# Performance work log

Measured on AMD Instinct MI355X. Metric: run time of the kernel, lower is better.

Reference implementation:

```python
import jax, jax.numpy as jnp
import numpy as np

B, N, C = 4, 262144, 10
K_PRE, K_POST = 4096, 500          # before_nms_max, after_nms_max
ROI_THR, NMS_THR = 0.1, 0.01       # roi_threshold, nms_threshold


def setup_inputs() -> dict:
    key = jax.random.key(0)
    k1, k2, k3, k4 = jax.random.split(key, 4)
    # raw logits; sigmoid(-2 + noise) straddles roi_threshold=0.1 realistically
    cls = jax.random.normal(k1, (B, N, C), jnp.float32) - 2.0
    centers = jax.random.uniform(k2, (B, N, 3), jnp.float32, minval=-50.0, maxval=50.0)
    sizes = jax.random.uniform(k3, (B, N, 3), jnp.float32, minval=0.5, maxval=5.0)
    heading = jax.random.uniform(k4, (B, N, 1), jnp.float32, minval=-np.pi, maxval=np.pi)
    boxes = jnp.concatenate([centers, sizes, heading], axis=-1)  # (B, N, 7)
    return {"batch_cls_preds": cls, "batch_box_preds": boxes}


def _pairwise_bev_iou(b):
    # b: (K, 7) = [x, y, z, dx, dy, dz, heading]; BEV IoU (heading ignored,
    # axis-aligned approximation of the rotated-IoU CUDA kernel).
    x, y, dx, dy = b[:, 0], b[:, 1], b[:, 3], b[:, 4]
    x1, x2 = x - dx * 0.5, x + dx * 0.5
    y1, y2 = y - dy * 0.5, y + dy * 0.5
    ix = jnp.clip(jnp.minimum(x2[:, None], x2[None, :]) - jnp.maximum(x1[:, None], x1[None, :]), 0.0)
    iy = jnp.clip(jnp.minimum(y2[:, None], y2[None, :]) - jnp.maximum(y1[:, None], y1[None, :]), 0.0)
    inter = ix * iy                              # (K, K)
    area = dx * dy                               # (K,)
    union = area[:, None] + area[None, :] - inter
    return inter / jnp.maximum(union, 1e-6)


def _nms_one(scores, labels, boxes):
    # scores: (N,), labels: (N,) int32, boxes: (N, 7)
    s = jnp.where(scores > ROI_THR, scores, -1.0)       # score-threshold filter
    topv, topi = jax.lax.top_k(s, K_PRE)                # keep top before_nms_max
    tb = boxes[topi]                                     # (K_PRE, 7)
    tl = labels[topi]
    iou = _pairwise_bev_iou(tb)                          # (K_PRE, K_PRE)
    keep0 = topv > ROI_THR

    def body(i, keep):
        # a kept higher-score box i suppresses later boxes with IoU > thr
        sup = (iou[i] > NMS_THR) & (jnp.arange(K_PRE) > i) & keep[i]
        return keep & ~sup

    keep = jax.lax.fori_loop(0, K_PRE, body, keep0)
    kept_scores = jnp.where(keep, topv, -1.0)
    fv, fi = jax.lax.top_k(kept_scores, K_POST)          # after_nms_max slots
    m = fv > 0.0
    final_scores = jnp.where(m, fv, 0.0)                 # (K_POST,)
    final_boxes = tb[fi] * m[:, None].astype(tb.dtype)   # (K_POST, 7)
    final_labels = jnp.where(m, tl[fi], -1)              # (K_POST,)
    return final_scores, final_boxes, final_labels


def reference(batch_cls_preds, batch_box_preds):
    probs = jax.nn.sigmoid(batch_cls_preds)              # (B, N, C)
    scores = jnp.max(probs, axis=-1)                     # per-anchor best class score
    labels = jnp.argmax(probs, axis=-1).astype(jnp.int32)
    final_scores, final_boxes, final_labels = jax.vmap(_nms_one)(scores, labels, batch_box_preds)
    return final_scores, final_boxes, final_labels
```

## Files before the change

kernel.cpp:

```cpp
#include <hip/hip_runtime.h>
#include <stdint.h>

constexpr int B = 4;
constexpr int N = 262144;
constexpr int C = 10;
constexpr int KPRE = 4096;
constexpr int KPOST = 500;
constexpr float ROI_THR = 0.1f;
constexpr float NMS_THR = 0.01f;
constexpr int CAP = 8192;
constexpr int MASKW = KPRE / 64;
constexpr int RJT = 2;
constexpr int MAXP = 32;

__device__ __forceinline__ uint32_t f2k(float f) {
  uint32_t u = __float_as_uint(f);
  return (u & 0x80000000u) ? ~u : (u | 0x80000000u);
}
__device__ __forceinline__ float k2f(uint32_t k) {
  uint32_t u = (k & 0x80000000u) ? (k ^ 0x80000000u) : ~k;
  return __uint_as_float(u);
}
__device__ __forceinline__ float sigm(float x) { return 1.0f / (1.0f + expf(-x)); }

__device__ __forceinline__ void async_lds16(const void* g, void* l) {
  __builtin_amdgcn_global_load_lds((const __attribute__((address_space(1))) void*)g,
                                   (__attribute__((address_space(3))) void*)l, 16, 0, 0);
}

__device__ __forceinline__ uint2 select256(const uint32_t* __restrict__ h, uint32_t R,
                                           uint32_t* s, uint32_t* o2) {
  int t = threadIdx.x;
  s[t] = h[t];
  __syncthreads();
  for (int off = 1; off < 256; off <<= 1) {
    uint32_t v = s[t] + ((t + off < 256) ? s[t + off] : 0u);
    __syncthreads();
    s[t] = v;
    __syncthreads();
  }
  uint32_t suf = s[t];
  uint32_t sufn = (t < 255) ? s[t + 1] : 0u;
  if (suf >= R && R > sufn) {
    o2[0] = (uint32_t)t;
    o2[1] = R - sufn;
  }
  __syncthreads();
  uint2 r;
  r.x = o2[0];
  r.y = o2[1];
  __syncthreads();
  return r;
}

__global__ void zeroK(uint32_t* __restrict__ p, int n) {
  int i = blockIdx.x * 256 + threadIdx.x;
  if (i < n) p[i] = 0u;
}

__global__ void scoreK(const float* __restrict__ cls, uint32_t* __restrict__ keys,
                       uint32_t* __restrict__ hist0, uint32_t* __restrict__ hist1) {
  __shared__ float ls[2560];
  __shared__ uint32_t h[256];
  __shared__ uint32_t h1[256];
  int b = blockIdx.y;
  int t = threadIdx.x;
  h[t] = 0;
  h1[t] = 0;
  size_t base = ((size_t)b * N + (size_t)blockIdx.x * 256) * C;
  const float2* g2 = (const float2*)(cls + base);
  float2* l2 = (float2*)ls;
#pragma unroll
  for (int r = 0; r < 5; ++r) l2[r * 256 + t] = g2[r * 256 + t];
  __syncthreads();
  const float* mine = ls + t * 10;
  float m = mine[0];
#pragma unroll
  for (int c = 1; c < C; ++c) m = fmaxf(m, mine[c]);
  float p = sigm(m);
  float sc = (p > ROI_THR) ? p : -1.0f;
  uint32_t k = f2k(sc);
  keys[(size_t)b * N + blockIdx.x * 256 + t] = k;
  atomicAdd(&h[k >> 24], 1u);
  if ((k >> 24) == 0xBFu) atomicAdd(&h1[(k >> 16) & 255u], 1u);
  __syncthreads();
  if (h[t]) atomicAdd(&hist0[b * 256 + t], h[t]);
  if (h1[t]) atomicAdd(&hist1[b * 256 + t], h1[t]);
}

__global__ void histP1K(const uint32_t* __restrict__ keys, const uint32_t* __restrict__ hist0,
                        uint32_t* __restrict__ hist1b) {
  __shared__ uint32_t s[256];
  __shared__ uint32_t o2[2];
  __shared__ uint32_t h[256];
  int b = blockIdx.y;
  int t = threadIdx.x;
  uint2 s0 = select256(hist0 + b * 256, (uint32_t)KPRE, s, o2);
  if (s0.x == 0xBFu) return;
  h[t] = 0;
  __syncthreads();
  uint32_t pref = s0.x;
  const uint4* kb4 = (const uint4*)(keys + (size_t)b * N);
#pragma unroll
  for (int r = 0; r < 2; ++r) {
    uint4 kv = kb4[blockIdx.x * 512 + r * 256 + t];
#pragma unroll
    for (int j = 0; j < 4; ++j) {
      uint32_t k = (&kv.x)[j];
      if ((k >> 24) == pref) atomicAdd(&h[(k >> 16) & 255u], 1u);
    }
  }
  __syncthreads();
  if (h[t]) atomicAdd(&hist1b[b * 256 + t], h[t]);
}

__global__ void compactK(const uint32_t* __restrict__ keys, const uint32_t* __restrict__ hist0,
                         const uint32_t* __restrict__ hist1, const uint32_t* __restrict__ hist1b,
                         unsigned long long* __restrict__ list, uint32_t* __restrict__ cnt) {
  __shared__ uint32_t s[256];
  __shared__ uint32_t o2[2];
  __shared__ uint32_t scan[256];
  __shared__ uint32_t baseSh;
  int b = blockIdx.y;
  int t = threadIdx.x;
  uint2 s0 = select256(hist0 + b * 256, (uint32_t)KPRE, s, o2);
  const uint32_t* h1 = (s0.x == 0xBFu) ? hist1 : hist1b;
  uint2 s1 = select256(h1 + b * 256, s0.y, s, o2);
  uint32_t T = ((s0.x << 8) | s1.x) << 16;
  const uint4* kb4 = (const uint4*)(keys + (size_t)b * N);
  uint4 kv[4];
#pragma unroll
  for (int r = 0; r < 4; ++r) kv[r] = kb4[blockIdx.x * 1024 + r * 256 + t];
  uint32_t c = 0;
#pragma unroll
  for (int r = 0; r < 4; ++r)
#pragma unroll
    for (int j = 0; j < 4; ++j) c += ((&kv[r].x)[j] >= T) ? 1u : 0u;
  scan[t] = c;
  __syncthreads();
  for (int off = 1; off < 256; off <<= 1) {
    uint32_t v = scan[t] + ((t >= off) ? scan[t - off] : 0u);
    __syncthreads();
    scan[t] = v;
    __syncthreads();
  }
  uint32_t excl = scan[t] - c;
  if (t == 255) baseSh = atomicAdd(&cnt[b], scan[255]);
  __syncthreads();
  uint32_t pos = baseSh + excl;
#pragma unroll
  for (int r = 0; r < 4; ++r)
#pragma unroll
    for (int j = 0; j < 4; ++j) {
      uint32_t k = (&kv[r].x)[j];
      if (k >= T) {
        uint32_t n = (blockIdx.x * 1024 + r * 256 + t) * 4 + j;
        if (pos < CAP)
          list[(size_t)b * CAP + pos] = ((unsigned long long)k << 32) | (uint32_t)(~n);
        pos++;
      }
    }
}

__global__ void rankK(const unsigned long long* __restrict__ list, const uint32_t* __restrict__ cnt,
                      uint32_t* __restrict__ rank) {
  __shared__ unsigned long long lp[256];
  int b = blockIdx.z;
  int cc = (int)min(cnt[b], (uint32_t)CAP);
  if (blockIdx.x * 256 >= cc) return;
  int j0 = blockIdx.y * (256 * RJT);
  if (j0 >= cc) return;
  int i = blockIdx.x * 256 + threadIdx.x;
  unsigned long long pi = (i < cc) ? list[(size_t)b * CAP + i] : ~0ull;
  uint32_t c = 0;
#pragma unroll
  for (int tb = 0; tb < RJT; ++tb) {
    int j = j0 + tb * 256 + threadIdx.x;
    __syncthreads();
    lp[threadIdx.x] = (j < cc) ? list[(size_t)b * CAP + j] : 0ull;
    __syncthreads();
#pragma unroll 8
    for (int jj = 0; jj < 256; ++jj) c += (lp[jj] > pi) ? 1u : 0u;
  }
  if (i < cc && c) atomicAdd(&rank[(size_t)b * CAP + i], c);
}

__global__ void scatterK(const unsigned long long* __restrict__ list,
                         const uint32_t* __restrict__ cnt, const uint32_t* __restrict__ rank,
                         const float* __restrict__ boxes, float* __restrict__ sel_score,
                         uint32_t* __restrict__ sel_idx, float* __restrict__ sel_box) {
  int b = blockIdx.y;
  int p = blockIdx.x * 256 + threadIdx.x;
  uint32_t cc = min(cnt[b], (uint32_t)CAP);
  if (p >= (int)cc) return;
  unsigned long long pk = list[(size_t)b * CAP + p];
  uint32_t r = rank[(size_t)b * CAP + p];
  if (r >= (uint32_t)KPRE) return;
  uint32_t key = (uint32_t)(pk >> 32);
  uint32_t idx = ~(uint32_t)pk;
  sel_score[b * KPRE + r] = k2f(key);
  sel_idx[b * KPRE + r] = idx;
  const float* src = boxes + ((size_t)b * N + idx) * 7;
  float* dst = sel_box + ((size_t)b * KPRE + r) * 8;
#pragma unroll
  for (int c = 0; c < 7; ++c) dst[c] = src[c];
  dst[7] = 0.f;
}

template <bool CHK>
__device__ __forceinline__ void mask_row64(int tt, const float4* __restrict__ jv,
                                           const float* __restrict__ ja, float x1i, float x2i,
                                           float y1i, float y2i, float ai, uint32_t& lo0,
                                           uint32_t& hi0, uint32_t& band) {
#pragma unroll 16
  for (int jj = 0; jj < 64; ++jj) {
    float4 v = jv[jj];
    float aj = ja[jj];
    float xx1 = fmaxf(x1i, v.x), xx2 = fminf(x2i, v.y);
    float yy1 = fmaxf(y1i, v.z), yy2 = fminf(y2i, v.w);
    float ix = fmaxf(__fsub_rn(xx2, xx1), 0.0f), iy = fmaxf(__fsub_rn(yy2, yy1), 0.0f);
    float inter = __fmul_rn(ix, iy);
    float den = fmaxf(__fsub_rn(__fadd_rn(ai, aj), inter), 1e-6f);
    float q0 = __fmul_rn(NMS_THR, den);
    float d = __fsub_rn(inter, q0);
    band |= (fabsf(d) <= __fmul_rn(q0, 1e-5f)) ? 1u : 0u;
    bool sup = d > 0.0f;
    if (CHK) sup = sup && (jj > tt);
    uint32_t bit = sup ? 1u : 0u;
    if (jj < 32) lo0 |= bit << jj; else hi0 |= bit << (jj - 32);
  }
}

__global__ __launch_bounds__(64) void maskK(const float* __restrict__ sel_box,
                                            unsigned long long* __restrict__ maskT,
                                            unsigned long long* __restrict__ Tmat) {
  int b = blockIdx.z;
  int bi = blockIdx.x;
  int w = blockIdx.y;
  if (w < bi) return;
  int t = threadIdx.x;
  int i = bi * 64 + t;
  int j0 = w * 64;
  __shared__ float4 jv[64];
  __shared__ float ja[64];
  {
    const float4* bj = (const float4*)(sel_box + ((size_t)b * KPRE + j0 + t) * 8);
    float4 lo = bj[0], hi = bj[1];
    float xj = lo.x, yj = lo.y, dxj = lo.w, dyj = hi.x;
    float hxj = __fmul_rn(dxj, 0.5f), hyj = __fmul_rn(dyj, 0.5f);
    float4 v;
    v.x = __fsub_rn(xj, hxj);
    v.y = __fadd_rn(xj, hxj);
    v.z = __fsub_rn(yj, hyj);
    v.w = __fadd_rn(yj, hyj);
    jv[t] = v;
    ja[t] = __fmul_rn(dxj, dyj);
  }
  __syncthreads();
  const float4* myb = (const float4*)(sel_box + ((size_t)b * KPRE + i) * 8);
  float4 lo = myb[0], hi = myb[1];
  float x = lo.x, y = lo.y, dx = lo.w, dy = hi.x;
  float hx = __fmul_rn(dx, 0.5f), hy = __fmul_rn(dy, 0.5f);
  float x1i = __fsub_rn(x, hx), x2i = __fadd_rn(x, hx);
  float y1i = __fsub_rn(y, hy), y2i = __fadd_rn(y, hy);
  float ai = __fmul_rn(dx, dy);
  uint32_t lo0 = 0, hi0 = 0, band = 0;
  if (w == bi)
    mask_row64<true>(t, jv, ja, x1i, x2i, y1i, y2i, ai, lo0, hi0, band);
  else
    mask_row64<false>(t, jv, ja, x1i, x2i, y1i, y2i, ai, lo0, hi0, band);
  if (__builtin_expect(__any(band != 0), 0)) {
    lo0 = hi0 = 0;
    for (int jj = 0; jj < 64; ++jj) {
      float4 v = jv[jj];
      float aj = ja[jj];
      float xx1 = fmaxf(x1i, v.x), xx2 = fminf(x2i, v.y);
      float yy1 = fmaxf(y1i, v.z), yy2 = fminf(y2i, v.w);
      float ix = fmaxf(__fsub_rn(xx2, xx1), 0.0f), iy = fmaxf(__fsub_rn(yy2, yy1), 0.0f);
      float inter = __fmul_rn(ix, iy);
      float den = fmaxf(__fsub_rn(__fadd_rn(ai, aj), inter), 1e-6f);
      bool sup = (inter / den) > NMS_THR && (j0 + jj > i);
      uint32_t bit = sup ? 1u : 0u;
      if (jj < 32) lo0 |= bit << jj; else hi0 |= bit << (jj - 32);
    }
  }
  unsigned long long wacc = ((unsigned long long)hi0 << 32) | lo0;
  maskT[((size_t)b * MASKW + w) * KPRE + i] = wacc;
  if (w == bi) {
    unsigned long long m = wacc;
    unsigned long long T = 0ull;
#pragma unroll
    for (int j = 0; j < 64; ++j) {
      unsigned long long bj = __ballot(((m >> j) & 1ull) != 0ull);
      if (t == j) T = bj;
    }
    unsigned long long* trow = Tmat + ((size_t)b * 64 + w) * 128;
    trow[t] = T;
    trow[64 + t] = m;
  }
}

__global__ void nmsK(const unsigned long long* __restrict__ maskT,
                     const unsigned long long* __restrict__ Tmat,
                     const float* __restrict__ sel_score,
                     uint32_t* __restrict__ kept_pos, uint32_t* __restrict__ kept_cnt) {
  __shared__ unsigned long long td[64][128];
  __shared__ uint32_t keptbuf[KPOST];
  int b = blockIdx.x;
  int t = threadIdx.x;

  const char* tsrc = (const char*)(Tmat + (size_t)b * 64 * 128);
  for (int g = 0; g < 64; ++g)
    async_lds16(tsrc + (size_t)g * 1024 + (size_t)t * 16, &td[g][0]);

  unsigned long long cand = 0ull;
  for (int k = 0; k < 64; ++k) {
    float s = sel_score[b * KPRE + k * 64 + t];
    unsigned long long bal = __ballot(s > ROI_THR);
    if (t == k) cand = bal;
  }
  asm volatile("s_waitcnt vmcnt(0)" ::: "memory");

  const unsigned long long* mbt = maskT + (size_t)b * KPRE * MASKW + (size_t)t * KPRE;
  unsigned long long remv = 0ull;
  unsigned long long r[MAXP];
#pragma unroll
  for (int a = 0; a < MAXP; ++a) r[a] = 0ull;
  int kc = 0;

  for (int g = 0; g < 64; ++g) {
#pragma unroll
    for (int a = 0; a < MAXP; ++a) remv |= r[a];

    unsigned long long cw = cand & ~remv;
    unsigned long long aw =
        ((unsigned long long)(uint32_t)__builtin_amdgcn_readlane((uint32_t)(cw >> 32), g) << 32) |
        (uint32_t)__builtin_amdgcn_readlane((uint32_t)cw, g);
    if (aw) {
      unsigned long long T = td[g][t];
      unsigned long long m = td[g][64 + t];
      unsigned long long K = __ballot((m & aw) != 0ull);
      unsigned long long alive = aw;
      unsigned long long rem = aw & K;
      if (rem) {
        bool deadf = ((aw >> t) & 1ull) == 0ull;
        while (rem) {
          int s = __ffsll((long long)rem) - 1;
          rem &= rem - 1ull;
          if ((alive >> s) & 1ull) {
            deadf = deadf || (((T >> s) & 1ull) != 0ull);
            alive = __ballot(!deadf);
            rem &= alive;
          }
        }
      }
      int grp = __popcll(alive);
      if ((alive >> t) & 1ull) {
        int rk = __popcll(alive & ((1ull << t) - 1ull));
        if (kc + rk < KPOST) keptbuf[kc + rk] = (uint32_t)(g * 64 + t);
      }
      kc += grp;
      unsigned long long a2 = alive;
      bool again = true;
      while (again) {
#pragma unroll
        for (int a = 0; a < MAXP; ++a) {
          if (a2) {
            int s2 = __ffsll((long long)a2) - 1;
            a2 &= a2 - 1ull;
            r[a] = (t >= g) ? mbt[g * 64 + s2] : 0ull;
          } else {
            r[a] = 0ull;
          }
        }
        if (a2) {
#pragma unroll
          for (int a = 0; a < MAXP; ++a) {
            remv |= r[a];
            r[a] = 0ull;
          }
          again = true;
        } else {
          again = false;
        }
      }
      if (kc >= KPOST) break;
    } else {
#pragma unroll
      for (int a = 0; a < MAXP; ++a) r[a] = 0ull;
    }
  }
  asm volatile("s_waitcnt vmcnt(0)" ::: "memory");
  int kcc = min(kc, KPOST);
  for (int i = t; i < kcc; i += 64) kept_pos[b * KPOST + i] = keptbuf[i];
  if (t == 0) kept_cnt[b] = (uint32_t)kcc;
}

__global__ void outK(const float* __restrict__ cls,
                     const float* __restrict__ sel_score, const uint32_t* __restrict__ sel_idx,
                     const float* __restrict__ sel_box,
                     const uint32_t* __restrict__ kept_pos, const uint32_t* __restrict__ kept_cnt,
                     float* __restrict__ out) {
  int b = blockIdx.y;
  int s = blockIdx.x * blockDim.x + threadIdx.x;
  if (s >= KPOST) return;
  float* oS = out;
  float* oB = out + B * KPOST;
  float* oL = out + B * KPOST + B * KPOST * 7;
  uint32_t kcnt = kept_cnt[b];
  if (s < (int)kcnt) {
    uint32_t pos = kept_pos[b * KPOST + s];
    oS[b * KPOST + s] = sel_score[b * KPRE + pos];
    const float* box = sel_box + ((size_t)b * KPRE + pos) * 8;
    float* dst = oB + ((size_t)b * KPOST + s) * 7;
#pragma unroll
    for (int c = 0; c < 7; ++c) dst[c] = box[c];
    uint32_t idx = sel_idx[b * KPRE + pos];
    const float* p = cls + ((size_t)b * N + idx) * C;
    float bestv = sigm(p[0]);
    int bestc = 0;
#pragma unroll
    for (int c = 1; c < C; ++c) {
      float v = sigm(p[c]);
      if (v > bestv) { bestv = v; bestc = c; }
    }
    oL[b * KPOST + s] = (float)bestc;
  } else {
    oS[b * KPOST + s] = 0.0f;
    float* dst = oB + ((size_t)b * KPOST + s) * 7;
#pragma unroll
    for (int c = 0; c < 7; ++c) dst[c] = 0.0f;
    oL[b * KPOST + s] = -1.0f;
  }
}

__global__ void sentinelK(float* out, int n) {
  int i = blockIdx.x * blockDim.x + threadIdx.x;
  if (i < n) out[i] = 1337.0f;
}

extern "C" void kernel_launch(void* const* d_in, const int* in_sizes, int n_in,
                              void* d_out, int out_size, void* d_ws, size_t ws_size,
                              hipStream_t stream) {
  const float* cls = (const float*)d_in[0];
  const float* boxes = (const float*)d_in[1];
  float* out = (float*)d_out;

  char* ws = (char*)d_ws;
  size_t off = 0;
  auto alloc = [&](size_t bytes) -> void* {
    void* p = ws + off;
    off = (off + bytes + 255) & ~(size_t)255;
    return p;
  };
  size_t mask_bytes = (size_t)B * KPRE * MASKW * 8;
  unsigned long long* mask = (unsigned long long*)alloc(mask_bytes);
  unsigned long long* list = (unsigned long long*)alloc((size_t)B * CAP * 8);
  uint32_t* keys = (uint32_t*)alloc((size_t)B * N * 4);
  float* sel_box = (float*)alloc((size_t)B * KPRE * 8 * 4);
  float* sel_score = (float*)alloc((size_t)B * KPRE * 4);
  uint32_t* sel_idx = (uint32_t*)alloc((size_t)B * KPRE * 4);
  uint32_t* kept_pos = (uint32_t*)alloc((size_t)B * KPOST * 4);
  uint32_t* kept_cnt = (uint32_t*)alloc(B * 4);
  unsigned long long* Tmat = (unsigned long long*)alloc((size_t)B * 64 * 128 * 8);

  uint32_t* hist0 = (uint32_t*)mask;
  uint32_t* hist1 = hist0 + B * 256;
  uint32_t* hist1b = hist1 + B * 256;
  uint32_t* cnt = hist1b + B * 256;
  uint32_t* rank = (uint32_t*)((char*)mask + 16384);
  int zwords = (16384 + B * CAP * 4) / 4;

  if (off > ws_size) {
    sentinelK<<<dim3((out_size + 255) / 256), 256, 0, stream>>>(out, out_size);
    return;
  }

  zeroK<<<dim3((zwords + 255) / 256), 256, 0, stream>>>((uint32_t*)mask, zwords);
  scoreK<<<dim3(N / 256, B), 256, 0, stream>>>(cls, keys, hist0, hist1);
  histP1K<<<dim3(N / 2048, B), 256, 0, stream>>>(keys, hist0, hist1b);
  compactK<<<dim3(N / 4096, B), 256, 0, stream>>>(keys, hist0, hist1, hist1b, list, cnt);
  rankK<<<dim3(CAP / 256, CAP / (256 * RJT), B), 256, 0, stream>>>(list, cnt, rank);
  scatterK<<<dim3(CAP / 256, B), 256, 0, stream>>>(list, cnt, rank, boxes, sel_score, sel_idx,
                                                   sel_box);
  maskK<<<dim3(64, 64, B), 64, 0, stream>>>(sel_box, mask, Tmat);
  nmsK<<<B, 64, 0, stream>>>(mask, Tmat, sel_score, kept_pos, kept_cnt);
  outK<<<dim3((KPOST + 255) / 256, B), 256, 0, stream>>>(cls, sel_score, sel_idx, sel_box,
                                                         kept_pos, kept_cnt, out);
}
```

Before: 150.9 us.

## Fuse rank with scatter via last-block counter, fold output into NMS, drop histogram pass

Removes the histP1K second-level histogram pass: when the top radix bucket is not 0xBF, the threshold now uses only the top byte, so more candidates may reach compaction. Rank and scatter are merged into one kernel, where the last j-chunk block for each i-tile (found with an atomic done counter) does the scatter. The output gather is folded into the single-wave-per-batch NMS kernel. The aim is fewer kernel launches and less inter-kernel idle time, at the cost of possible CAP overflow when the coarser threshold is used, and a serial 64-thread output loop.

```diff
diff --git a/kernel.cpp b/kernel.cpp
--- a/kernel.cpp
+++ b/kernel.cpp
@@ -11,6 +11,7 @@
 constexpr int CAP = 8192;
 constexpr int MASKW = KPRE / 64;
 constexpr int RJT = 2;
+constexpr int NJCH = CAP / (256 * RJT);
 constexpr int MAXP = 32;
 
 __device__ __forceinline__ uint32_t f2k(float f) {
@@ -88,34 +89,8 @@
   if (h1[t]) atomicAdd(&hist1[b * 256 + t], h1[t]);
 }
 
-__global__ void histP1K(const uint32_t* __restrict__ keys, const uint32_t* __restrict__ hist0,
-                        uint32_t* __restrict__ hist1b) {
-  __shared__ uint32_t s[256];
-  __shared__ uint32_t o2[2];
-  __shared__ uint32_t h[256];
-  int b = blockIdx.y;
-  int t = threadIdx.x;
-  uint2 s0 = select256(hist0 + b * 256, (uint32_t)KPRE, s, o2);
-  if (s0.x == 0xBFu) return;
-  h[t] = 0;
-  __syncthreads();
-  uint32_t pref = s0.x;
-  const uint4* kb4 = (const uint4*)(keys + (size_t)b * N);
-#pragma unroll
-  for (int r = 0; r < 2; ++r) {
-    uint4 kv = kb4[blockIdx.x * 512 + r * 256 + t];
-#pragma unroll
-    for (int j = 0; j < 4; ++j) {
-      uint32_t k = (&kv.x)[j];
-      if ((k >> 24) == pref) atomicAdd(&h[(k >> 16) & 255u], 1u);
-    }
-  }
-  __syncthreads();
-  if (h[t]) atomicAdd(&hist1b[b * 256 + t], h[t]);
-}
-
 __global__ void compactK(const uint32_t* __restrict__ keys, const uint32_t* __restrict__ hist0,
-                         const uint32_t* __restrict__ hist1, const uint32_t* __restrict__ hist1b,
+                         const uint32_t* __restrict__ hist1,
                          unsigned long long* __restrict__ list, uint32_t* __restrict__ cnt) {
   __shared__ uint32_t s[256];
   __shared__ uint32_t o2[2];
@@ -124,9 +99,13 @@
   int b = blockIdx.y;
   int t = threadIdx.x;
   uint2 s0 = select256(hist0 + b * 256, (uint32_t)KPRE, s, o2);
-  const uint32_t* h1 = (s0.x == 0xBFu) ? hist1 : hist1b;
-  uint2 s1 = select256(h1 + b * 256, s0.y, s, o2);
-  uint32_t T = ((s0.x << 8) | s1.x) << 16;
+  uint32_t T;
+  if (s0.x == 0xBFu) {
+    uint2 s1 = select256(hist1 + b * 256, s0.y, s, o2);
+    T = ((s0.x << 8) | s1.x) << 16;
+  } else {
+    T = s0.x << 24;
+  }
   const uint4* kb4 = (const uint4*)(keys + (size_t)b * N);
   uint4 kv[4];
 #pragma unroll
@@ -162,49 +141,53 @@
     }
 }
 
-__global__ void rankK(const unsigned long long* __restrict__ list, const uint32_t* __restrict__ cnt,
-                      uint32_t* __restrict__ rank) {
+__global__ void rankscatK(const unsigned long long* __restrict__ list,
+                          const uint32_t* __restrict__ cnt, uint32_t* __restrict__ rank,
+                          uint32_t* __restrict__ done, const float* __restrict__ boxes,
+                          float* __restrict__ sel_score, uint32_t* __restrict__ sel_idx,
+                          float* __restrict__ sel_box) {
   __shared__ unsigned long long lp[256];
+  __shared__ uint32_t lastSh;
   int b = blockIdx.z;
+  int itile = blockIdx.x;
+  int t = threadIdx.x;
   int cc = (int)min(cnt[b], (uint32_t)CAP);
-  if (blockIdx.x * 256 >= cc) return;
-  int j0 = blockIdx.y * (256 * RJT);
-  if (j0 >= cc) return;
-  int i = blockIdx.x * 256 + threadIdx.x;
-  unsigned long long pi = (i < cc) ? list[(size_t)b * CAP + i] : ~0ull;
-  uint32_t c = 0;
-#pragma unroll
-  for (int tb = 0; tb < RJT; ++tb) {
-    int j = j0 + tb * 256 + threadIdx.x;
-    __syncthreads();
-    lp[threadIdx.x] = (j < cc) ? list[(size_t)b * CAP + j] : 0ull;
-    __syncthreads();
+  int i = itile * 256 + t;
+  if (itile * 256 < cc) {
+    int j0 = blockIdx.y * (256 * RJT);
+    if (j0 < cc) {
+      unsigned long long pi = (i < cc) ? list[(size_t)b * CAP + i] : ~0ull;
+      uint32_t c = 0;
+#pragma unroll
+      for (int tb = 0; tb < RJT; ++tb) {
+        int j = j0 + tb * 256 + t;
+        __syncthreads();
+        lp[t] = (j < cc) ? list[(size_t)b * CAP + j] : 0ull;
+        __syncthreads();
 #pragma unroll 8
-    for (int jj = 0; jj < 256; ++jj) c += (lp[jj] > pi) ? 1u : 0u;
-  }
-  if (i < cc && c) atomicAdd(&rank[(size_t)b * CAP + i], c);
-}
-
-__global__ void scatterK(const unsigned long long* __restrict__ list,
-                         const uint32_t* __restrict__ cnt, const uint32_t* __restrict__ rank,
-                         const float* __restrict__ boxes, float* __restrict__ sel_score,
-                         uint32_t* __restrict__ sel_idx, float* __restrict__ sel_box) {
-  int b = blockIdx.y;
-  int p = blockIdx.x * 256 + threadIdx.x;
-  uint32_t cc = min(cnt[b], (uint32_t)CAP);
-  if (p >= (int)cc) return;
-  unsigned long long pk = list[(size_t)b * CAP + p];
-  uint32_t r = rank[(size_t)b * CAP + p];
-  if (r >= (uint32_t)KPRE) return;
-  uint32_t key = (uint32_t)(pk >> 32);
-  uint32_t idx = ~(uint32_t)pk;
-  sel_score[b * KPRE + r] = k2f(key);
-  sel_idx[b * KPRE + r] = idx;
-  const float* src = boxes + ((size_t)b * N + idx) * 7;
-  float* dst = sel_box + ((size_t)b * KPRE + r) * 8;
-#pragma unroll
-  for (int c = 0; c < 7; ++c) dst[c] = src[c];
-  dst[7] = 0.f;
+        for (int jj = 0; jj < 256; ++jj) c += (lp[jj] > pi) ? 1u : 0u;
+      }
+      if (i < cc && c) atomicAdd(&rank[(size_t)b * CAP + i], c);
+    }
+  }
+  __syncthreads();
+  if (t == 0) lastSh = atomicAdd(&done[b * 32 + itile], 1u);
+  __syncthreads();
+  if (lastSh == NJCH - 1 && i < cc) {
+    unsigned long long pk = list[(size_t)b * CAP + i];
+    uint32_t r = atomicAdd(&rank[(size_t)b * CAP + i], 0u);
+    if (r < (uint32_t)KPRE) {
+      uint32_t key = (uint32_t)(pk >> 32);
+      uint32_t idx = ~(uint32_t)pk;
+      sel_score[b * KPRE + r] = k2f(key);
+      sel_idx[b * KPRE + r] = idx;
+      const float* src = boxes + ((size_t)b * N + idx) * 7;
+      float* dst = sel_box + ((size_t)b * KPRE + r) * 8;
+#pragma unroll
+      for (int c7 = 0; c7 < 7; ++c7) dst[c7] = src[c7];
+      dst[7] = 0.f;
+    }
+  }
 }
 
 template <bool CHK>
@@ -300,10 +283,12 @@
   }
 }
 
-__global__ void nmsK(const unsigned long long* __restrict__ maskT,
-                     const unsigned long long* __restrict__ Tmat,
-                     const float* __restrict__ sel_score,
-                     uint32_t* __restrict__ kept_pos, uint32_t* __restrict__ kept_cnt) {
+__global__ void nmsoutK(const unsigned long long* __restrict__ maskT,
+                        const unsigned long long* __restrict__ Tmat,
+                        const float* __restrict__ sel_score,
+                        const uint32_t* __restrict__ sel_idx,
+                        const float* __restrict__ sel_box, const float* __restrict__ cls,
+                        float* __restrict__ out) {
   __shared__ unsigned long long td[64][128];
   __shared__ uint32_t keptbuf[KPOST];
   int b = blockIdx.x;
@@ -392,45 +377,35 @@
   }
   asm volatile("s_waitcnt vmcnt(0)" ::: "memory");
   int kcc = min(kc, KPOST);
-  for (int i = t; i < kcc; i += 64) kept_pos[b * KPOST + i] = keptbuf[i];
-  if (t == 0) kept_cnt[b] = (uint32_t)kcc;
-}
-
-__global__ void outK(const float* __restrict__ cls,
-                     const float* __restrict__ sel_score, const uint32_t* __restrict__ sel_idx,
-                     const float* __restrict__ sel_box,
-                     const uint32_t* __restrict__ kept_pos, const uint32_t* __restrict__ kept_cnt,
-                     float* __restrict__ out) {
-  int b = blockIdx.y;
-  int s = blockIdx.x * blockDim.x + threadIdx.x;
-  if (s >= KPOST) return;
+
   float* oS = out;
   float* oB = out + B * KPOST;
   float* oL = out + B * KPOST + B * KPOST * 7;
-  uint32_t kcnt = kept_cnt[b];
-  if (s < (int)kcnt) {
-    uint32_t pos = kept_pos[b * KPOST + s];
-    oS[b * KPOST + s] = sel_score[b * KPRE + pos];
-    const float* box = sel_box + ((size_t)b * KPRE + pos) * 8;
-    float* dst = oB + ((size_t)b * KPOST + s) * 7;
-#pragma unroll
-    for (int c = 0; c < 7; ++c) dst[c] = box[c];
-    uint32_t idx = sel_idx[b * KPRE + pos];
-    const float* p = cls + ((size_t)b * N + idx) * C;
-    float bestv = sigm(p[0]);
-    int bestc = 0;
-#pragma unroll
-    for (int c = 1; c < C; ++c) {
-      float v = sigm(p[c]);
-      if (v > bestv) { bestv = v; bestc = c; }
-    }
-    oL[b * KPOST + s] = (float)bestc;
-  } else {
-    oS[b * KPOST + s] = 0.0f;
-    float* dst = oB + ((size_t)b * KPOST + s) * 7;
-#pragma unroll
-    for (int c = 0; c < 7; ++c) dst[c] = 0.0f;
-    oL[b * KPOST + s] = -1.0f;
+  for (int s = t; s < KPOST; s += 64) {
+    if (s < kcc) {
+      uint32_t pos = keptbuf[s];
+      oS[b * KPOST + s] = sel_score[b * KPRE + pos];
+      const float* box = sel_box + ((size_t)b * KPRE + pos) * 8;
+      float* dst = oB + ((size_t)b * KPOST + s) * 7;
+#pragma unroll
+      for (int c = 0; c < 7; ++c) dst[c] = box[c];
+      uint32_t idx = sel_idx[b * KPRE + pos];
+      const float* p = cls + ((size_t)b * N + idx) * C;
+      float bestv = sigm(p[0]);
+      int bestc = 0;
+#pragma unroll
+      for (int c = 1; c < C; ++c) {
+        float v = sigm(p[c]);
+        if (v > bestv) { bestv = v; bestc = c; }
+      }
+      oL[b * KPOST + s] = (float)bestc;
+    } else {
+      oS[b * KPOST + s] = 0.0f;
+      float* dst = oB + ((size_t)b * KPOST + s) * 7;
+#pragma unroll
+      for (int c = 0; c < 7; ++c) dst[c] = 0.0f;
+      oL[b * KPOST + s] = -1.0f;
+    }
   }
 }
 
@@ -460,14 +435,12 @@
   float* sel_box = (float*)alloc((size_t)B * KPRE * 8 * 4);
   float* sel_score = (float*)alloc((size_t)B * KPRE * 4);
   uint32_t* sel_idx = (uint32_t*)alloc((size_t)B * KPRE * 4);
-  uint32_t* kept_pos = (uint32_t*)alloc((size_t)B * KPOST * 4);
-  uint32_t* kept_cnt = (uint32_t*)alloc(B * 4);
   unsigned long long* Tmat = (unsigned long long*)alloc((size_t)B * 64 * 128 * 8);
 
   uint32_t* hist0 = (uint32_t*)mask;
   uint32_t* hist1 = hist0 + B * 256;
-  uint32_t* hist1b = hist1 + B * 256;
-  uint32_t* cnt = hist1b + B * 256;
+  uint32_t* cnt = hist1 + B * 256;
+  uint32_t* done = cnt + B;
   uint32_t* rank = (uint32_t*)((char*)mask + 16384);
   int zwords = (16384 + B * CAP * 4) / 4;
 
@@ -478,13 +451,9 @@
 
   zeroK<<<dim3((zwords + 255) / 256), 256, 0, stream>>>((uint32_t*)mask, zwords);
   scoreK<<<dim3(N / 256, B), 256, 0, stream>>>(cls, keys, hist0, hist1);
-  histP1K<<<dim3(N / 2048, B), 256, 0, stream>>>(keys, hist0, hist1b);
-  compactK<<<dim3(N / 4096, B), 256, 0, stream>>>(keys, hist0, hist1, hist1b, list, cnt);
-  rankK<<<dim3(CAP / 256, CAP / (256 * RJT), B), 256, 0, stream>>>(list, cnt, rank);
-  scatterK<<<dim3(CAP / 256, B), 256, 0, stream>>>(list, cnt, rank, boxes, sel_score, sel_idx,
-                                                   sel_box);
+  compactK<<<dim3(N / 4096, B), 256, 0, stream>>>(keys, hist0, hist1, list, cnt);
+  rankscatK<<<dim3(CAP / 256, NJCH, B), 256, 0, stream>>>(list, cnt, rank, done, boxes, sel_score,
+                                                          sel_idx, sel_box);
   maskK<<<dim3(64, 64, B), 64, 0, stream>>>(sel_box, mask, Tmat);
-  nmsK<<<B, 64, 0, stream>>>(mask, Tmat, sel_score, kept_pos, kept_cnt);
-  outK<<<dim3((KPOST + 255) / 256, B), 256, 0, stream>>>(cls, sel_score, sel_idx, sel_box,
-                                                         kept_pos, kept_cnt, out);
-}
+  nmsoutK<<<B, 64, 0, stream>>>(mask, Tmat, sel_score, sel_idx, sel_box, cls, out);
+}
```

After: 154.6 us. 1.02x slower.
